# Kernel tuning notes

Hardware: AMD Instinct MI355X
Metric: run time of the kernel (lower is better)

The kernel has to match this reference:

```python
import jax, jax.numpy as jnp
import numpy as np

N, S, D = 4, 2048, 1024
H, HD = 16, 64
DF = 3 * D
EPS = 1e-5

def _layernorm(x, g, b):
    mu = jnp.mean(x, axis=-1, keepdims=True)
    var = jnp.mean((x - mu) ** 2, axis=-1, keepdims=True)
    return (x - mu) * jax.lax.rsqrt(var + EPS) * g + b

def _pos_embed(s, d, dtype):
    pos = jnp.arange(s, dtype=dtype)                      # (S,)
    i = jnp.arange(d, dtype=dtype)                        # (D,)
    ang = pos[:, None] / (10000.0 ** (2.0 * i / d))       # (S,D)
    pe = jnp.where((jnp.arange(d) % 2) == 0, jnp.sin(ang), jnp.cos(ang))
    return pe

def setup_inputs() -> dict:
    key = jax.random.key(0)
    ks = jax.random.split(key, 12)
    def w(k, shape, fan_in):
        return jax.random.normal(k, shape, dtype=jnp.float32) * (fan_in ** -0.5)
    return {
        "x":  jax.random.normal(ks[0], (N, S, D), dtype=jnp.float32),
        "Wq": w(ks[1], (D, H * HD), D),
        "Wk": w(ks[2], (D, H * HD), D),
        "Wv": w(ks[3], (D, H * HD), D),
        "Wo": w(ks[4], (H * HD, D), H * HD),
        "W1": w(ks[5], (D, DF), D),
        "b1": jnp.zeros((DF,), dtype=jnp.float32),
        "W2": w(ks[6], (DF, D), DF),
        "b2": jnp.zeros((D,), dtype=jnp.float32),
        "g1": jnp.ones((D,), dtype=jnp.float32),
        "be1": jnp.zeros((D,), dtype=jnp.float32),
        "g2": jnp.ones((D,), dtype=jnp.float32),
        "be2": jnp.zeros((D,), dtype=jnp.float32),
    }

def reference(x, Wq, Wk, Wv, Wo, W1, b1, W2, b2, g1, be1, g2, be2):
    n, s, d = x.shape
    # positional encoding (added to x; note original scales scores by model_dim**0.5)
    x = x + _pos_embed(s, d, x.dtype)[None, :, :]
    # MHA on norm1(x)
    h = _layernorm(x, g1, be1)
    q = (h @ Wq).reshape(n, s, H, HD)
    k = (h @ Wk).reshape(n, s, H, HD)
    v = (h @ Wv).reshape(n, s, H, HD)
    scores = jnp.einsum('bqhd,bkhd->bhqk', q, k) / jnp.sqrt(jnp.asarray(d, x.dtype))
    attn = jax.nn.softmax(scores, axis=-1)
    o = jnp.einsum('bhqk,bkhd->bqhd', attn, v).reshape(n, s, H * HD)
    x = x + o @ Wo
    # FFN on norm2(x): Linear -> LeakyReLU(0.01) -> Linear (dropout = identity in eval)
    h2 = _layernorm(x, g2, be2)
    f = jax.nn.leaky_relu(h2 @ W1 + b1, negative_slope=0.01)
    x = x + (f @ W2 + b2)
    return x
```

## Files before the change

### kernel.cpp

```cpp
#include <hip/hip_runtime.h>

typedef unsigned short u16;
typedef __bf16 bf16x8 __attribute__((ext_vector_type(8)));
typedef float f32x4 __attribute__((ext_vector_type(4)));

__device__ __forceinline__ u16 f2bf(float f) {
  unsigned u = __builtin_bit_cast(unsigned, f);
  u += 0x7FFFu + ((u >> 16) & 1u);
  return (u16)(u >> 16);
}

#define GLOAD16(g, l) __builtin_amdgcn_global_load_lds( \
    (const __attribute__((address_space(1))) unsigned int*)(const void*)(g), \
    (__attribute__((address_space(3))) unsigned int*)(void*)(l), 16, 0, 0)

#define SW(r, c) (((r) << 6) + ((((c) ^ ((r) & 7))) << 3))

__global__ __launch_bounds__(256) void tconv(const float* __restrict__ W,
                                             u16* __restrict__ Wt, int K, int N) {
  __shared__ float t[32][33];
  int n0 = blockIdx.x * 32, k0 = blockIdx.y * 32;
  int tx = threadIdx.x, ty = threadIdx.y;
#pragma unroll
  for (int j = 0; j < 4; ++j)
    t[ty + j * 8][tx] = W[(size_t)(k0 + ty + j * 8) * N + n0 + tx];
  __syncthreads();
#pragma unroll
  for (int j = 0; j < 4; ++j)
    Wt[(size_t)(n0 + ty + j * 8) * K + k0 + tx] = f2bf(t[tx][ty + j * 8]);
}

template <bool PE>
__global__ __launch_bounds__(256) void ln_row(const float* __restrict__ in,
                                              const float* __restrict__ g,
                                              const float* __restrict__ be,
                                              float* __restrict__ xout,
                                              u16* __restrict__ hout) {
  const int row = blockIdx.x;
  const int tid = threadIdx.x;
  const int s = row & 2047;
  float4 xv = *(const float4*)&in[(size_t)row * 1024 + tid * 4];
  float vals[4];
  const float* xp = (const float*)&xv;
#pragma unroll
  for (int j = 0; j < 4; ++j) {
    float v = xp[j];
    if (PE) {
      int d = tid * 4 + j;
      float freq = powf(10000.f, -2.f * (float)d * (1.f / 1024.f));
      float ang = (float)s * freq;
      v += (d & 1) ? cosf(ang) : sinf(ang);
    }
    vals[j] = v;
  }
  if (PE) {
    float4 st;
    float* sp = (float*)&st;
#pragma unroll
    for (int j = 0; j < 4; ++j) sp[j] = vals[j];
    *(float4*)&xout[(size_t)row * 1024 + tid * 4] = st;
  }
  float sum = vals[0] + vals[1] + vals[2] + vals[3];
  float sq = vals[0] * vals[0] + vals[1] * vals[1] + vals[2] * vals[2] + vals[3] * vals[3];
#pragma unroll
  for (int d = 1; d < 64; d <<= 1) {
    sum += __shfl_xor(sum, d);
    sq += __shfl_xor(sq, d);
  }
  __shared__ float red[8];
  int wave = tid >> 6, lane = tid & 63;
  if (lane == 0) { red[wave] = sum; red[4 + wave] = sq; }
  __syncthreads();
  sum = red[0] + red[1] + red[2] + red[3];
  sq = red[4] + red[5] + red[6] + red[7];
  float mu = sum * (1.f / 1024.f);
  float var = sq * (1.f / 1024.f) - mu * mu;
  float rv = rsqrtf(var + 1e-5f);
#pragma unroll
  for (int j = 0; j < 4; ++j) {
    int d = tid * 4 + j;
    hout[(size_t)row * 1024 + d] = f2bf((vals[j] - mu) * rv * g[d] + be[d]);
  }
}

#define EPI_QKV 0
#define EPI_OPROJ 1
#define EPI_FFN1 2
#define EPI_FFN2 3

template <int EPI>
__global__ __launch_bounds__(256, 2) void gemm_bt(
    const u16* __restrict__ A, const u16* __restrict__ Bt, int M, int N, int K,
    const float* __restrict__ bias, const float* __restrict__ resid,
    float* __restrict__ outf, u16* __restrict__ outb,
    u16* __restrict__ oq, u16* __restrict__ okk, u16* __restrict__ ovt) {
  __shared__ __align__(16) u16 As[128 * 64];
  __shared__ __align__(16) u16 Bs[128 * 64];
  const int tid = threadIdx.x;
  const int wave = tid >> 6, lane = tid & 63;
  const int m0 = blockIdx.y * 128, n0 = blockIdx.x * 128;
  const int lrow = lane & 15, lhi = lane >> 4;
  const int wr = (wave >> 1) * 64, wc = (wave & 1) * 64;
  const int srow = tid >> 3;
  const int swsrc = ((tid & 7) ^ (srow & 7)) * 8;
  const u16* Ag = A + (size_t)(m0 + srow) * K + swsrc;
  const u16* Bg = Bt + (size_t)(n0 + srow) * K + swsrc;

  f32x4 acc[4][4] = {};

  for (int kt = 0; kt < K; kt += 64) {
#pragma unroll
    for (int j = 0; j < 4; ++j) {
      GLOAD16(Ag + (size_t)(j * 32) * K + kt, &As[j * 2048 + wave * 512]);
      GLOAD16(Bg + (size_t)(j * 32) * K + kt, &Bs[j * 2048 + wave * 512]);
    }
    __syncthreads();
    bf16x8 af[2][4], bfr[2][4];
#pragma unroll
    for (int kk = 0; kk < 2; ++kk) {
#pragma unroll
      for (int m = 0; m < 4; ++m)
        af[kk][m] = *(const bf16x8*)&As[SW(wr + m * 16 + lrow, kk * 4 + lhi)];
#pragma unroll
      for (int n = 0; n < 4; ++n)
        bfr[kk][n] = *(const bf16x8*)&Bs[SW(wc + n * 16 + lrow, kk * 4 + lhi)];
    }
#pragma unroll
    for (int kk = 0; kk < 2; ++kk)
#pragma unroll
      for (int m = 0; m < 4; ++m)
#pragma unroll
        for (int n = 0; n < 4; ++n)
          acc[m][n] = __builtin_amdgcn_mfma_f32_16x16x32_bf16(af[kk][m], bfr[kk][n], acc[m][n], 0, 0, 0);
    __syncthreads();
  }

#pragma unroll
  for (int m = 0; m < 4; ++m) {
#pragma unroll
    for (int n = 0; n < 4; ++n) {
#pragma unroll
      for (int i = 0; i < 4; ++i) {
        int row = m0 + wr + m * 16 + lhi * 4 + i;
        int col = n0 + wc + n * 16 + lrow;
        float v = acc[m][n][i];
        if (EPI == EPI_QKV) {
          int which = col >> 10, c = col & 1023;
          int h = c >> 6, hd = c & 63;
          int b = row >> 11, s = row & 2047;
          size_t qk = (((size_t)(b * 16 + h) * 2048 + s) << 6) + hd;
          if (which == 0) oq[qk] = f2bf(v * 0.03125f);
          else if (which == 1) okk[qk] = f2bf(v);
          else ovt[((size_t)(b * 16 + h) * 64 + hd) * 2048 + s] = f2bf(v);
        } else if (EPI == EPI_OPROJ) {
          size_t idx = (size_t)row * 1024 + col;
          outf[idx] = v + resid[idx];
        } else if (EPI == EPI_FFN1) {
          float t = v + bias[col];
          t = t > 0.f ? t : 0.01f * t;
          outb[(size_t)row * 3072 + col] = f2bf(t);
        } else {
          size_t idx = (size_t)row * 1024 + col;
          outf[idx] = v + bias[col] + resid[idx];
        }
      }
    }
  }
}

__global__ __launch_bounds__(256, 3) void attn_fwd(const u16* __restrict__ qb,
                                                   const u16* __restrict__ kbuf,
                                                   const u16* __restrict__ vtb,
                                                   u16* __restrict__ ob) {
  __shared__ __align__(16) u16 Kl[2][64 * 64];
  __shared__ __align__(16) u16 Vl[2][64 * 64];
  __shared__ __align__(16) u16 Pl[128 * 64];
  const int tid = threadIdx.x, wave = tid >> 6, lane = tid & 63;
  const int wid = (blockIdx.x & 7) * 128 + (blockIdx.x >> 3);
  const int bh = wid >> 4, qt = wid & 15;
  const int lrow = lane & 15, lhi = lane >> 4;
  const u16* Qg = qb + (((size_t)bh * 2048 + qt * 128) << 6);
  const u16* Kg = kbuf + ((size_t)bh * 2048 << 6);
  const u16* Vg = vtb + (size_t)bh * 64 * 2048;
  const int srow = tid >> 3;
  const int swsrc = ((tid & 7) ^ (srow & 7)) * 8;

#pragma unroll
  for (int j = 0; j < 4; ++j)
    GLOAD16(Qg + (size_t)(srow + j * 32) * 64 + swsrc, &Pl[j * 2048 + wave * 512]);
#pragma unroll
  for (int j = 0; j < 2; ++j) {
    int r = srow + j * 32;
    GLOAD16(Kg + (size_t)r * 64 + swsrc, &Kl[0][j * 2048 + wave * 512]);
    GLOAD16(Vg + (size_t)r * 2048 + swsrc, &Vl[0][j * 2048 + wave * 512]);
  }
  __syncthreads();

  bf16x8 qf[2][2];
#pragma unroll
  for (int m = 0; m < 2; ++m)
#pragma unroll
    for (int kk = 0; kk < 2; ++kk)
      qf[m][kk] = *(const bf16x8*)&Pl[SW(wave * 32 + m * 16 + lrow, kk * 4 + lhi)];

  f32x4 oacc[2][4] = {};
  float lsum[8];
#pragma unroll
  for (int i = 0; i < 8; ++i) lsum[i] = 0.f;

  int cur = 0;
  for (int kv = 0; kv < 2048; kv += 64) {
    if (kv) __syncthreads();
    if (kv + 64 < 2048) {
#pragma unroll
      for (int j = 0; j < 2; ++j) {
        int r = srow + j * 32;
        GLOAD16(Kg + (size_t)(kv + 64 + r) * 64 + swsrc, &Kl[cur ^ 1][j * 2048 + wave * 512]);
        GLOAD16(Vg + (size_t)r * 2048 + kv + 64 + swsrc, &Vl[cur ^ 1][j * 2048 + wave * 512]);
      }
    }

    f32x4 sf[2][4] = {};
#pragma unroll
    for (int n = 0; n < 4; ++n) {
#pragma unroll
      for (int kk = 0; kk < 2; ++kk) {
        bf16x8 kf = *(const bf16x8*)&Kl[cur][SW(n * 16 + lrow, kk * 4 + lhi)];
        sf[0][n] = __builtin_amdgcn_mfma_f32_16x16x32_bf16(qf[0][kk], kf, sf[0][n], 0, 0, 0);
        sf[1][n] = __builtin_amdgcn_mfma_f32_16x16x32_bf16(qf[1][kk], kf, sf[1][n], 0, 0, 0);
      }
    }
#pragma unroll
    for (int m = 0; m < 2; ++m) {
#pragma unroll
      for (int i = 0; i < 4; ++i) {
        float rs = 0.f;
#pragma unroll
        for (int n = 0; n < 4; ++n) {
          float p = __expf(sf[m][n][i]);
          sf[m][n][i] = p;
          rs += p;
        }
        lsum[m * 4 + i] += rs;
      }
    }
#pragma unroll
    for (int m = 0; m < 2; ++m)
#pragma unroll
      for (int n = 0; n < 4; ++n)
#pragma unroll
        for (int i = 0; i < 4; ++i) {
          int pr = wave * 32 + m * 16 + lhi * 4 + i;
          Pl[SW(pr, n * 2 + (lrow >> 3)) + (lrow & 7)] = f2bf(sf[m][n][i]);
        }
#pragma unroll
    for (int kk = 0; kk < 2; ++kk) {
      bf16x8 pf0 = *(const bf16x8*)&Pl[SW(wave * 32 + 0 + lrow, kk * 4 + lhi)];
      bf16x8 pf1 = *(const bf16x8*)&Pl[SW(wave * 32 + 16 + lrow, kk * 4 + lhi)];
#pragma unroll
      for (int n = 0; n < 4; ++n) {
        bf16x8 vf = *(const bf16x8*)&Vl[cur][SW(n * 16 + lrow, kk * 4 + lhi)];
        oacc[0][n] = __builtin_amdgcn_mfma_f32_16x16x32_bf16(pf0, vf, oacc[0][n], 0, 0, 0);
        oacc[1][n] = __builtin_amdgcn_mfma_f32_16x16x32_bf16(pf1, vf, oacc[1][n], 0, 0, 0);
      }
    }
    cur ^= 1;
  }

#pragma unroll
  for (int idx = 0; idx < 8; ++idx)
#pragma unroll
    for (int d = 1; d < 16; d <<= 1)
      lsum[idx] += __shfl_xor(lsum[idx], d, 16);

  const int b = bh >> 4, h = bh & 15;
#pragma unroll
  for (int m = 0; m < 2; ++m)
#pragma unroll
    for (int i = 0; i < 4; ++i) {
      int qrow = qt * 128 + wave * 32 + m * 16 + lhi * 4 + i;
      float inv = 1.f / lsum[m * 4 + i];
#pragma unroll
      for (int n = 0; n < 4; ++n) {
        int hd = n * 16 + lrow;
        ob[((size_t)(b * 2048 + qrow)) * 1024 + h * 64 + hd] = f2bf(oacc[m][n][i] * inv);
      }
    }
}

extern "C" void kernel_launch(void* const* d_in, const int* in_sizes, int n_in,
                              void* d_out, int out_size, void* d_ws, size_t ws_size,
                              hipStream_t stream) {
  const float* x = (const float*)d_in[0];
  const float* Wq = (const float*)d_in[1];
  const float* Wk = (const float*)d_in[2];
  const float* Wv = (const float*)d_in[3];
  const float* Wo = (const float*)d_in[4];
  const float* W1 = (const float*)d_in[5];
  const float* b1 = (const float*)d_in[6];
  const float* W2 = (const float*)d_in[7];
  const float* b2 = (const float*)d_in[8];
  const float* g1 = (const float*)d_in[9];
  const float* be1 = (const float*)d_in[10];
  const float* g2 = (const float*)d_in[11];
  const float* be2 = (const float*)d_in[12];

  char* ws = (char*)d_ws;
  const size_t MB = 1024 * 1024;
  float* x1 = (float*)(ws + 0);
  u16* h = (u16*)(ws + 32 * MB);
  u16* q = (u16*)(ws + 48 * MB);
  u16* k = (u16*)(ws + 64 * MB);
  u16* vt = (u16*)(ws + 80 * MB);
  u16* o = (u16*)(ws + 96 * MB);
  u16* f = (u16*)(ws + 48 * MB);
  u16* wqkv = (u16*)(ws + 112 * MB);
  u16* wo = (u16*)(ws + 118 * MB);
  u16* w1t = (u16*)(ws + 120 * MB);
  u16* w2t = (u16*)(ws + 126 * MB);
  float* out = (float*)d_out;

  dim3 tb(32, 8);
  tconv<<<dim3(32, 32), tb, 0, stream>>>(Wq, wqkv, 1024, 1024);
  tconv<<<dim3(32, 32), tb, 0, stream>>>(Wk, wqkv + 1024 * 1024, 1024, 1024);
  tconv<<<dim3(32, 32), tb, 0, stream>>>(Wv, wqkv + 2 * 1024 * 1024, 1024, 1024);
  tconv<<<dim3(32, 32), tb, 0, stream>>>(Wo, wo, 1024, 1024);
  tconv<<<dim3(96, 32), tb, 0, stream>>>(W1, w1t, 1024, 3072);
  tconv<<<dim3(32, 96), tb, 0, stream>>>(W2, w2t, 3072, 1024);

  ln_row<true><<<8192, 256, 0, stream>>>(x, g1, be1, x1, h);

  gemm_bt<EPI_QKV><<<dim3(24, 64), 256, 0, stream>>>(h, wqkv, 8192, 3072, 1024,
                                                     nullptr, nullptr, nullptr, nullptr,
                                                     q, k, vt);
  attn_fwd<<<1024, 256, 0, stream>>>(q, k, vt, o);

  gemm_bt<EPI_OPROJ><<<dim3(8, 64), 256, 0, stream>>>(o, wo, 8192, 1024, 1024,
                                                      nullptr, x1, x1, nullptr,
                                                      nullptr, nullptr, nullptr);
  ln_row<false><<<8192, 256, 0, stream>>>(x1, g2, be2, nullptr, h);

  gemm_bt<EPI_FFN1><<<dim3(24, 64), 256, 0, stream>>>(h, w1t, 8192, 3072, 1024,
                                                      b1, nullptr, nullptr, f,
                                                      nullptr, nullptr, nullptr);
  gemm_bt<EPI_FFN2><<<dim3(8, 64), 256, 0, stream>>>(f, w2t, 8192, 1024, 3072,
                                                     b2, x1, out, nullptr,
                                                     nullptr, nullptr, nullptr);
}
```

Measured before the change: 433.8 us.

## Transpose score MFMA so each lane owns a query row, pack P writes

Swaps the MFMA operands for QK^T so each lane holds four consecutive key scores for one query row. This allows packed bf16 conversion (v_cvt_pk_bf16_f32) and 8-byte LDS stores of P instead of scalar 2-byte stores. Folds log2(e) into the Q scale so exp2f replaces __expf. The row-sum reduction shrinks from 8 accumulators with 16-lane shuffles to 2 accumulators with two cross-half shuffles plus a broadcast at the end. The aim is fewer LDS store instructions, fewer conversions and less shuffle work in the attention inner loop.

Measured after the change: 436.1 us. About the same (+0.5%).

```diff
diff --git a/kernel.cpp b/kernel.cpp
--- a/kernel.cpp
+++ b/kernel.cpp
@@ -15,6 +15,8 @@
     (__attribute__((address_space(3))) unsigned int*)(void*)(l), 16, 0, 0)
 
 #define SW(r, c) (((r) << 6) + ((((c) ^ ((r) & 7))) << 3))
+
+#define QSCALE 0.045084222393f
 
 __global__ __launch_bounds__(256) void tconv(const float* __restrict__ W,
                                              u16* __restrict__ Wt, int K, int N) {
@@ -149,7 +151,7 @@
           int h = c >> 6, hd = c & 63;
           int b = row >> 11, s = row & 2047;
           size_t qk = (((size_t)(b * 16 + h) * 2048 + s) << 6) + hd;
-          if (which == 0) oq[qk] = f2bf(v * 0.03125f);
+          if (which == 0) oq[qk] = f2bf(v * QSCALE);
           else if (which == 1) okk[qk] = f2bf(v);
           else ovt[((size_t)(b * 16 + h) * 64 + hd) * 2048 + s] = f2bf(v);
         } else if (EPI == EPI_OPROJ) {
@@ -204,9 +206,7 @@
       qf[m][kk] = *(const bf16x8*)&Pl[SW(wave * 32 + m * 16 + lrow, kk * 4 + lhi)];
 
   f32x4 oacc[2][4] = {};
-  float lsum[8];
-#pragma unroll
-  for (int i = 0; i < 8; ++i) lsum[i] = 0.f;
+  float lsum[2] = {0.f, 0.f};
 
   int cur = 0;
   for (int kv = 0; kv < 2048; kv += 64) {
@@ -226,33 +226,33 @@
 #pragma unroll
       for (int kk = 0; kk < 2; ++kk) {
         bf16x8 kf = *(const bf16x8*)&Kl[cur][SW(n * 16 + lrow, kk * 4 + lhi)];
-        sf[0][n] = __builtin_amdgcn_mfma_f32_16x16x32_bf16(qf[0][kk], kf, sf[0][n], 0, 0, 0);
-        sf[1][n] = __builtin_amdgcn_mfma_f32_16x16x32_bf16(qf[1][kk], kf, sf[1][n], 0, 0, 0);
+        sf[0][n] = __builtin_amdgcn_mfma_f32_16x16x32_bf16(kf, qf[0][kk], sf[0][n], 0, 0, 0);
+        sf[1][n] = __builtin_amdgcn_mfma_f32_16x16x32_bf16(kf, qf[1][kk], sf[1][n], 0, 0, 0);
       }
     }
 #pragma unroll
     for (int m = 0; m < 2; ++m) {
-#pragma unroll
-      for (int i = 0; i < 4; ++i) {
-        float rs = 0.f;
-#pragma unroll
-        for (int n = 0; n < 4; ++n) {
-          float p = __expf(sf[m][n][i]);
-          sf[m][n][i] = p;
-          rs += p;
-        }
-        lsum[m * 4 + i] += rs;
-      }
-    }
-#pragma unroll
-    for (int m = 0; m < 2; ++m)
-#pragma unroll
-      for (int n = 0; n < 4; ++n)
-#pragma unroll
-        for (int i = 0; i < 4; ++i) {
-          int pr = wave * 32 + m * 16 + lhi * 4 + i;
-          Pl[SW(pr, n * 2 + (lrow >> 3)) + (lrow & 7)] = f2bf(sf[m][n][i]);
-        }
+      const int pr = wave * 32 + m * 16 + lrow;
+      const int prbase = pr << 6;
+      float rs = 0.f;
+#pragma unroll
+      for (int n = 0; n < 4; ++n) {
+        float p0 = exp2f(sf[m][n][0]);
+        float p1 = exp2f(sf[m][n][1]);
+        float p2 = exp2f(sf[m][n][2]);
+        float p3 = exp2f(sf[m][n][3]);
+        rs += (p0 + p1) + (p2 + p3);
+        unsigned lo, hi;
+        asm("v_cvt_pk_bf16_f32 %0, %1, %2" : "=v"(lo) : "v"(p0), "v"(p1));
+        asm("v_cvt_pk_bf16_f32 %0, %1, %2" : "=v"(hi) : "v"(p2), "v"(p3));
+        const int chunk = (n * 2 + (lhi >> 1)) ^ (pr & 7);
+        uint2 pk;
+        pk.x = lo;
+        pk.y = hi;
+        *(uint2*)&Pl[prbase + (chunk << 3) + ((lhi & 1) << 2)] = pk;
+      }
+      lsum[m] += rs;
+    }
 #pragma unroll
     for (int kk = 0; kk < 2; ++kk) {
       bf16x8 pf0 = *(const bf16x8*)&Pl[SW(wave * 32 + 0 + lrow, kk * 4 + lhi)];
@@ -268,18 +268,19 @@
   }
 
 #pragma unroll
-  for (int idx = 0; idx < 8; ++idx)
-#pragma unroll
-    for (int d = 1; d < 16; d <<= 1)
-      lsum[idx] += __shfl_xor(lsum[idx], d, 16);
+  for (int m = 0; m < 2; ++m) {
+    lsum[m] += __shfl_xor(lsum[m], 16);
+    lsum[m] += __shfl_xor(lsum[m], 32);
+  }
 
   const int b = bh >> 4, h = bh & 15;
 #pragma unroll
   for (int m = 0; m < 2; ++m)
 #pragma unroll
     for (int i = 0; i < 4; ++i) {
+      float lq = __shfl(lsum[m], lhi * 4 + i, 64);
+      float inv = 1.f / lq;
       int qrow = qt * 128 + wave * 32 + m * 16 + lhi * 4 + i;
-      float inv = 1.f / lsum[m * 4 + i];
 #pragma unroll
       for (int n = 0; n < 4; ++n) {
         int hd = n * 16 + lrow;
```
